# Kernel tuning notes

Hardware: AMD Instinct MI355X
Metric: run time of the kernel (lower is better)

The kernel has to match this reference:

```python
import jax, jax.numpy as jnp
import numpy as np

N = 100000
E = 800000
D_IN = 128
D_H = 128
D_OUT = 40
L = 16
ALPHA = 0.1
THETA = 0.5
BN_EPS = 1e-5


def setup_inputs() -> dict:
    key = jax.random.key(0)
    ks = jax.random.split(key, 8)
    x = jax.random.normal(ks[0], (N, D_IN), dtype=jnp.float32)
    edge_row = jax.random.randint(ks[1], (E,), 0, N, dtype=jnp.int32)
    edge_col = jax.random.randint(ks[2], (E,), 0, N, dtype=jnp.int32)
    edge_weight = jax.random.uniform(ks[3], (E,), dtype=jnp.float32) / 8.0  # ~normalized adj values
    W_in = jax.random.normal(ks[4], (D_IN, D_H), dtype=jnp.float32) / np.sqrt(D_IN)
    b_in = jnp.zeros((D_H,), jnp.float32)
    conv_W = jax.random.normal(ks[5], (L, D_H, D_H), dtype=jnp.float32) / np.sqrt(D_H)
    bn_gamma = jnp.ones((L, D_H), jnp.float32)
    bn_beta = jnp.zeros((L, D_H), jnp.float32)
    W_out = jax.random.normal(ks[6], (D_H, D_OUT), dtype=jnp.float32) / np.sqrt(D_H)
    b_out = jnp.zeros((D_OUT,), jnp.float32)
    return {"x": x, "edge_weight": edge_weight, "W_in": W_in, "b_in": b_in,
            "conv_W": conv_W, "bn_gamma": bn_gamma, "bn_beta": bn_beta,
            "W_out": W_out, "b_out": b_out,
            "edge_row": edge_row, "edge_col": edge_col}


def reference(x, edge_weight, W_in, b_in, conv_W, bn_gamma, bn_beta, W_out, b_out, edge_row, edge_col):
    # input linear + relu (dropout p=0 -> identity)
    x0 = jax.nn.relu(x @ W_in + b_in)            # [N, D_H]
    # GCN2Conv beta coefficients: log(theta/layer + 1), layer = 1..L
    betas = jnp.log(THETA / jnp.arange(1, L + 1, dtype=jnp.float32) + 1.0)

    def spmm(h):
        # out[i] = sum_{e: row[e]=i} w[e] * h[col[e]]
        msgs = edge_weight[:, None] * h[edge_col]     # [E, D_H]
        return jax.ops.segment_sum(msgs, edge_row, num_segments=N)

    def layer(h, params):
        W, g, bb, beta = params
        a = spmm(h)                                   # propagate
        a = (1.0 - ALPHA) * a + ALPHA * x0            # initial-residual mix
        a = (1.0 - beta) * a + beta * (a @ W)         # shared-weights identity mapping
        mu = jnp.mean(a, axis=0)                      # BatchNorm1d (training stats)
        var = jnp.var(a, axis=0)
        a = (a - mu) * jax.lax.rsqrt(var + BN_EPS) * g + bb
        a = a + h                                     # residual
        return jax.nn.relu(a), None

    xL, _ = jax.lax.scan(layer, x0, (conv_W, bn_gamma, bn_beta, betas))
    return xL @ W_out + b_out                         # [N, D_OUT]
```

## Files before the change

kernel.cpp:

```cpp
#include <hip/hip_runtime.h>
#include <math.h>

#define NN 100000
#define EE 800000
#define DH 128
#define NL 16
#define GEMM_GRID 1563
#define SG_GRID 782
#define NSLOT 32
#define WROWS 12500

typedef __bf16 bf16x8 __attribute__((ext_vector_type(8)));
typedef float f32x4 __attribute__((ext_vector_type(4)));

__global__ void k_hist(const int* __restrict__ row, int* __restrict__ cnt) {
    int e = blockIdx.x * 256 + threadIdx.x;
    if (e < EE) atomicAdd(&cnt[row[e]], 1);
}

__global__ void k_scan1(const int* __restrict__ cnt, int* __restrict__ rp, int* __restrict__ part) {
    __shared__ int buf[512];
    int tid = threadIdx.x;
    int i = blockIdx.x * 512 + tid;
    int v = (i < NN) ? cnt[i] : 0;
    buf[tid] = v;
    __syncthreads();
    for (int off = 1; off < 512; off <<= 1) {
        int x = (tid >= off) ? buf[tid - off] : 0;
        __syncthreads();
        buf[tid] += x;
        __syncthreads();
    }
    if (i < NN) rp[i] = buf[tid] - v;
    if (tid == 511) part[blockIdx.x] = buf[511];
}

__global__ void k_scan2(int* __restrict__ part, int nparts) {
    __shared__ int buf[256];
    int tid = threadIdx.x;
    int v = (tid < nparts) ? part[tid] : 0;
    buf[tid] = v;
    __syncthreads();
    for (int off = 1; off < 256; off <<= 1) {
        int x = (tid >= off) ? buf[tid - off] : 0;
        __syncthreads();
        buf[tid] += x;
        __syncthreads();
    }
    if (tid < nparts) part[tid] = buf[tid] - v;
}

__global__ void k_scan3(int* __restrict__ rp, const int* __restrict__ part) {
    int i = blockIdx.x * 512 + threadIdx.x;
    if (i < NN) rp[i] += part[blockIdx.x];
    if (i == 0) rp[NN] = EE;
}

__global__ void k_dhist(const int* __restrict__ cnt, int* __restrict__ dbin) {
    __shared__ int lb[64];
    int tid = threadIdx.x;
    if (tid < 64) lb[tid] = 0;
    __syncthreads();
    int i = blockIdx.x * 256 + tid;
    if (i < NN) {
        int d = cnt[i];
        if (d > 63) d = 63;
        atomicAdd(&lb[63 - d], 1);
    }
    __syncthreads();
    if (tid < 64 && lb[tid]) atomicAdd(&dbin[tid], lb[tid]);
}

__global__ void k_pscan(const int* __restrict__ dbin, int* __restrict__ dpre) {
    if (threadIdx.x == 0) {
        int s = 0;
        for (int i = 0; i < 64; ++i) { dpre[i] = s; s += dbin[i]; }
    }
}

__global__ void k_pscatter(const int* __restrict__ cnt, const int* __restrict__ dpre,
                           int* __restrict__ dfil, int* __restrict__ perm) {
    __shared__ int lcnt[64], lbase[64];
    int tid = threadIdx.x;
    if (tid < 64) lcnt[tid] = 0;
    __syncthreads();
    int i = blockIdx.x * 256 + tid;
    int b = 0, loc = 0;
    bool ok = (i < NN);
    if (ok) {
        int d = cnt[i];
        if (d > 63) d = 63;
        b = 63 - d;
        loc = atomicAdd(&lcnt[b], 1);
    }
    __syncthreads();
    if (tid < 64 && lcnt[tid]) lbase[tid] = atomicAdd(&dfil[tid], lcnt[tid]);
    __syncthreads();
    if (ok) perm[dpre[b] + lbase[b] + loc] = i;
}

__global__ void k_fill(const int* __restrict__ row, const int* __restrict__ col,
                       const float* __restrict__ w, const int* __restrict__ rp,
                       int* __restrict__ fil, int2* __restrict__ ep) {
    int b = blockIdx.x;
    int win = b & 7;
    int e = (b >> 3) * 256 + threadIdx.x;
    if (e >= EE) return;
    int r = row[e];
    if (r / WROWS != win) return;
    int pos = rp[r] + atomicAdd(&fil[r], 1);
    ep[pos] = make_int2(col[e], __float_as_int(0.9f * w[e]));
}

__global__ void k_prep_w(const float* __restrict__ convW, const float* __restrict__ Win,
                         __bf16* __restrict__ Bhi, __bf16* __restrict__ Blo) {
    int l = blockIdx.x;
    const float* W;
    float beta, ob;
    if (l < NL) {
        beta = logf(0.5f / (float)(l + 1) + 1.0f);
        ob = 1.0f - beta;
        W = convW + (size_t)l * DH * DH;
    } else {
        beta = 1.0f;
        ob = 0.0f;
        W = Win;
    }
    __bf16* bh = Bhi + (size_t)l * DH * DH;
    __bf16* bl = Blo + (size_t)l * DH * DH;
    for (int i = threadIdx.x; i < DH * DH; i += 256) {
        int k = i >> 7, j = i & 127;
        float v = beta * W[i] + ((k == j) ? ob : 0.f);
        __bf16 hv = (__bf16)v;
        int t = j >> 4, n = j & 15, ks = k >> 5, quad = (k >> 3) & 3, e = k & 7;
        int off = ((t * 4 + ks) * 64 + quad * 16 + n) * 8 + e;
        bh[off] = hv;
        bl[off] = (__bf16)(v - (float)hv);
    }
}

__global__ void k_prep_out(const float* __restrict__ Wout, __bf16* __restrict__ Bhi, __bf16* __restrict__ Blo) {
    for (int i = threadIdx.x; i < DH * 48; i += 256) {
        int k = i / 48, j = i % 48;
        float v = (j < 40) ? Wout[k * 40 + j] : 0.f;
        __bf16 hv = (__bf16)v;
        int t = j >> 4, n = j & 15, ks = k >> 5, quad = (k >> 3) & 3, e = k & 7;
        int off = ((t * 4 + ks) * 64 + quad * 16 + n) * 8 + e;
        Bhi[off] = hv;
        Blo[off] = (__bf16)(v - (float)hv);
    }
}

__device__ inline void split8(const float* p, bf16x8& hi, bf16x8& lo) {
    f32x4 v0 = *(const f32x4*)p;
    f32x4 v1 = *(const f32x4*)(p + 4);
#pragma unroll
    for (int j = 0; j < 4; ++j) {
        __bf16 h0 = (__bf16)v0[j];
        hi[j] = h0;
        lo[j] = (__bf16)(v0[j] - (float)h0);
        __bf16 h1 = (__bf16)v1[j];
        hi[4 + j] = h1;
        lo[4 + j] = (__bf16)(v1[j] - (float)h1);
    }
}

#define MFMA(a, b, c) __builtin_amdgcn_mfma_f32_16x16x32_bf16(a, b, c, 0, 0, 0)

__device__ inline float dec_scale(unsigned int sc4, int ks) {
    return __uint_as_float(((sc4 >> (8 * ks)) & 0xffu) << 23);
}

#define DEC_DW(dw, wsv, a0, a1, a2, a3)                         \
    {                                                           \
        a0 = fmaf(wsv, (float)((dw)&0xffu), a0);                \
        a1 = fmaf(wsv, (float)(((dw) >> 8) & 0xffu), a1);       \
        a2 = fmaf(wsv, (float)(((dw) >> 16) & 0xffu), a2);      \
        a3 = fmaf(wsv, (float)((dw) >> 24), a3);                \
    }

#define EDGE_FMA(S4, W, RA, RB)                                       \
    {                                                                 \
        float _w = (W);                                               \
        float _w0 = _w * dec_scale(S4, 0);                            \
        float _w1 = _w * dec_scale(S4, 1);                            \
        float _w2 = _w * dec_scale(S4, 2);                            \
        float _w3 = _w * dec_scale(S4, 3);                            \
        sw0 += _w0; sw1 += _w1; sw2 += _w2; sw3 += _w3;               \
        DEC_DW((RA).x, _w0, acc[0][0], acc[0][1], acc[0][2], acc[0][3]); \
        DEC_DW((RA).y, _w0, acc[0][4], acc[0][5], acc[0][6], acc[0][7]); \
        DEC_DW((RA).z, _w1, acc[1][0], acc[1][1], acc[1][2], acc[1][3]); \
        DEC_DW((RA).w, _w1, acc[1][4], acc[1][5], acc[1][6], acc[1][7]); \
        DEC_DW((RB).x, _w2, acc[2][0], acc[2][1], acc[2][2], acc[2][3]); \
        DEC_DW((RB).y, _w2, acc[2][4], acc[2][5], acc[2][6], acc[2][7]); \
        DEC_DW((RB).z, _w3, acc[3][0], acc[3][1], acc[3][2], acc[3][3]); \
        DEC_DW((RB).w, _w3, acc[3][4], acc[3][5], acc[3][6], acc[3][7]); \
    }

__global__ void k_cvt8(const __bf16* __restrict__ src, unsigned char* __restrict__ q8,
                       unsigned char* __restrict__ sc) {
    int t = blockIdx.x * 256 + threadIdx.x;
    if (t >= NN * 4) return;
    int node = t >> 2, ks = t & 3;
    const __bf16* p = src + (size_t)node * DH + ks * 32;
    float v[32];
    float mx = 0.f;
#pragma unroll
    for (int i = 0; i < 4; ++i) {
        bf16x8 b = *(const bf16x8*)(p + i * 8);
#pragma unroll
        for (int c = 0; c < 8; ++c) {
            float f = (float)b[c];
            v[i * 8 + c] = f;
            mx = fmaxf(mx, fabsf(f));
        }
    }
    unsigned int em = (__float_as_uint(mx) >> 23) & 0xffu;
    unsigned int eb;
    float sinv;
    if (em < 7) { eb = 0; sinv = 0.f; }
    else { eb = em - 6; sinv = __uint_as_float((254 - eb) << 23); }
    sc[(size_t)node * 4 + ks] = (unsigned char)eb;
    unsigned char* bp = q8 + (size_t)node * 128 + (ks >> 1) * 64 + (ks & 1) * 8;
#pragma unroll
    for (int q = 0; q < 4; ++q) {
        uint2 w;
        w.x = 0; w.y = 0;
#pragma unroll
        for (int c = 0; c < 4; ++c) {
            unsigned int q0 = (unsigned int)rintf(fminf(fmaf(v[q * 8 + c], sinv, 128.f), 255.f));
            unsigned int q1 = (unsigned int)rintf(fminf(fmaf(v[q * 8 + 4 + c], sinv, 128.f), 255.f));
            w.x |= q0 << (8 * c);
            w.y |= q1 << (8 * c);
        }
        *(uint2*)(bp + q * 16) = w;
    }
}

__global__ __launch_bounds__(512, 4) void k_spmm_gemm(const unsigned char* __restrict__ hin8,
                                                      const unsigned char* __restrict__ hinsc,
                                                      const unsigned char* __restrict__ x08,
                                                      const unsigned char* __restrict__ x0sc,
                                                      const int* __restrict__ rp, const int2* __restrict__ ep,
                                                      const int* __restrict__ perm,
                                                      __bf16* __restrict__ aout,
                                                      const __bf16* __restrict__ Bhi, const __bf16* __restrict__ Blo,
                                                      float* __restrict__ stats32) {
    __shared__ __bf16 Bs[2 * DH * DH];
    __shared__ float red[2][8][DH];
    int tid = threadIdx.x;
    {
        const f32x4* sh = (const f32x4*)Bhi;
        const f32x4* sl = (const f32x4*)Blo;
        f32x4* dh = (f32x4*)Bs;
        f32x4* dl = (f32x4*)(Bs + DH * DH);
#pragma unroll
        for (int i = 0; i < 4; ++i) {
            dh[tid + i * 512] = sh[tid + i * 512];
            dl[tid + i * 512] = sl[tid + i * 512];
        }
    }

    int wave = tid >> 6, lane = tid & 63;
    int n = lane & 15, quad = lane >> 4;
    int r0 = blockIdx.x * 128 + wave * 16;
    int idx = r0 + n;
    int pidx = (idx < NN) ? idx : (NN - 1);
    int node = perm[pidx];

    float acc[4][8];
#pragma unroll
    for (int ks = 0; ks < 4; ++ks)
#pragma unroll
        for (int c = 0; c < 8; ++c) acc[ks][c] = 0.f;
    float sw0 = 0.f, sw1 = 0.f, sw2 = 0.f, sw3 = 0.f;

    unsigned xs4 = *(const unsigned*)&x0sc[(size_t)node * 4];
    const unsigned char* xb = x08 + (size_t)node * 128 + quad * 16;
    uint4 xa = *(const uint4*)xb;
    uint4 xc = *(const uint4*)(xb + 64);

    int s = 0, e = 0;
    if (idx < NN) { s = rp[node]; e = rp[node + 1]; }
    int cnt = e - s;
    int npairs = cnt >> 1;

    const unsigned char* hb = hin8 + quad * 16;

    int2 cP0, cP1, fP0, fP1;
    unsigned cS0, cS1;
    uint4 cA0, cB0, cA1, cB1;
    if (npairs > 0) {
        cP0 = ep[s]; cP1 = ep[s + 1];
        cS0 = *(const unsigned*)&hinsc[(size_t)cP0.x * 4];
        cS1 = *(const unsigned*)&hinsc[(size_t)cP1.x * 4];
        const unsigned char* b0 = hb + (size_t)cP0.x * 128;
        const unsigned char* b1 = hb + (size_t)cP1.x * 128;
        cA0 = *(const uint4*)b0; cB0 = *(const uint4*)(b0 + 64);
        cA1 = *(const uint4*)b1; cB1 = *(const uint4*)(b1 + 64);
        int jf = s + 2; if (jf > EE - 2) jf = EE - 2;
        fP0 = ep[jf]; fP1 = ep[jf + 1];
    }

    EDGE_FMA(xs4, 0.1f, xa, xc);

    int j = s;
    for (int it = 0; it < npairs; ++it) {
        int j2 = j + 4; if (j2 > EE - 2) j2 = EE - 2;
        int2 eN0 = ep[j2], eN1 = ep[j2 + 1];
        unsigned tS0 = *(const unsigned*)&hinsc[(size_t)fP0.x * 4];
        unsigned tS1 = *(const unsigned*)&hinsc[(size_t)fP1.x * 4];
        const unsigned char* b0 = hb + (size_t)fP0.x * 128;
        const unsigned char* b1 = hb + (size_t)fP1.x * 128;
        uint4 tA0 = *(const uint4*)b0, tB0 = *(const uint4*)(b0 + 64);
        uint4 tA1 = *(const uint4*)b1, tB1 = *(const uint4*)(b1 + 64);
        EDGE_FMA(cS0, __int_as_float(cP0.y), cA0, cB0);
        EDGE_FMA(cS1, __int_as_float(cP1.y), cA1, cB1);
        cP0 = fP0; cP1 = fP1; fP0 = eN0; fP1 = eN1;
        cS0 = tS0; cS1 = tS1;
        cA0 = tA0; cB0 = tB0; cA1 = tA1; cB1 = tB1;
        j += 2;
    }
    if (cnt & 1) {
        int2 pe = ep[e - 1];
        unsigned s4 = *(const unsigned*)&hinsc[(size_t)pe.x * 4];
        const unsigned char* bp = hb + (size_t)pe.x * 128;
        uint4 ra = *(const uint4*)bp, rb = *(const uint4*)(bp + 64);
        EDGE_FMA(s4, __int_as_float(pe.y), ra, rb);
    }

    bf16x8 av[4];
    {
        float sws[4] = {sw0, sw1, sw2, sw3};
#pragma unroll
        for (int ks = 0; ks < 4; ++ks)
#pragma unroll
            for (int c = 0; c < 8; ++c)
                av[ks][c] = (__bf16)(acc[ks][c] - 128.0f * sws[ks]);
    }

    int prow[4];
#pragma unroll
    for (int r = 0; r < 4; ++r) prow[r] = __shfl(node, quad * 4 + r);

    __syncthreads();

    f32x4 gacc[8];
#pragma unroll
    for (int t = 0; t < 8; ++t) gacc[t] = (f32x4){0.f, 0.f, 0.f, 0.f};

#pragma unroll
    for (int ks = 0; ks < 4; ++ks) {
#pragma unroll
        for (int t = 0; t < 8; ++t) {
            int base = ((t * 4 + ks) * 64 + lane) * 8;
            bf16x8 bh = *(const bf16x8*)&Bs[base];
            bf16x8 bl = *(const bf16x8*)&Bs[DH * DH + base];
            gacc[t] = MFMA(av[ks], bh, gacc[t]);
            gacc[t] = MFMA(av[ks], bl, gacc[t]);
        }
    }

#pragma unroll
    for (int t = 0; t < 8; ++t) {
        float sm = 0.f, qq = 0.f;
#pragma unroll
        for (int r = 0; r < 4; ++r) {
            int row = r0 + quad * 4 + r;
            float v = gacc[t][r];
            if (row < NN) {
                aout[(size_t)prow[r] * DH + t * 16 + n] = (__bf16)v;
                sm += v;
                qq += v * v;
            }
        }
        sm += __shfl_xor(sm, 16); sm += __shfl_xor(sm, 32);
        qq += __shfl_xor(qq, 16); qq += __shfl_xor(qq, 32);
        if (quad == 0) {
            red[0][wave][t * 16 + n] = sm;
            red[1][wave][t * 16 + n] = qq;
        }
    }
    __syncthreads();
    if (tid < 256) {
        int which = tid >> 7, jj = tid & 127;
        float tot = 0.f;
#pragma unroll
        for (int w = 0; w < 8; ++w) tot += red[which][w][jj];
        atomicAdd(&stats32[(size_t)(blockIdx.x & (NSLOT - 1)) * 256 + tid], tot);
    }
}

__global__ __launch_bounds__(256) void k_lin_in(const float* __restrict__ X,
                                                const __bf16* __restrict__ Bhi, const __bf16* __restrict__ Blo,
                                                const float* __restrict__ bin, __bf16* __restrict__ x0) {
    __shared__ __bf16 Bs[2 * DH * DH];
    int tid = threadIdx.x;
    {
        const f32x4* sh = (const f32x4*)Bhi;
        const f32x4* sl = (const f32x4*)Blo;
        f32x4* dh = (f32x4*)Bs;
        f32x4* dl = (f32x4*)(Bs + DH * DH);
#pragma unroll
        for (int i = 0; i < 8; ++i) {
            dh[tid + i * 256] = sh[tid + i * 256];
            dl[tid + i * 256] = sl[tid + i * 256];
        }
    }
    __syncthreads();

    int wave = tid >> 6, lane = tid & 63;
    int n = lane & 15, quad = lane >> 4;
    int r0 = blockIdx.x * 64 + wave * 16;
    int arow = r0 + n;
    if (arow > NN - 1) arow = NN - 1;
    const float* pa = X + (size_t)arow * DH + quad * 8;

    f32x4 acc[8];
#pragma unroll
    for (int t = 0; t < 8; ++t) acc[t] = (f32x4){0.f, 0.f, 0.f, 0.f};

#pragma unroll
    for (int ks = 0; ks < 4; ++ks) {
        bf16x8 ah, al;
        split8(pa + ks * 32, ah, al);
#pragma unroll
        for (int t = 0; t < 8; ++t) {
            int base = ((t * 4 + ks) * 64 + lane) * 8;
            bf16x8 bh = *(const bf16x8*)&Bs[base];
            bf16x8 bl = *(const bf16x8*)&Bs[DH * DH + base];
            acc[t] = MFMA(ah, bh, acc[t]);
            acc[t] = MFMA(al, bh, acc[t]);
            acc[t] = MFMA(ah, bl, acc[t]);
        }
    }

#pragma unroll
    for (int t = 0; t < 8; ++t) {
        float bj = bin[t * 16 + n];
#pragma unroll
        for (int r = 0; r < 4; ++r) {
            int row = r0 + quad * 4 + r;
            if (row < NN) {
                float v = fmaxf(acc[t][r] + bj, 0.f);
                x0[(size_t)row * DH + t * 16 + n] = (__bf16)v;
            }
        }
    }
}

__global__ __launch_bounds__(256) void k_gemm_out(const __bf16* __restrict__ A,
                                                  const __bf16* __restrict__ Bhi, const __bf16* __restrict__ Blo,
                                                  const float* __restrict__ bout, float* __restrict__ out) {
    __shared__ __bf16 Bs[2 * 48 * DH];
    int tid = threadIdx.x;
    {
        const f32x4* sh = (const f32x4*)Bhi;
        const f32x4* sl = (const f32x4*)Blo;
        f32x4* dh = (f32x4*)Bs;
        f32x4* dl = (f32x4*)(Bs + 48 * DH);
#pragma unroll
        for (int i = 0; i < 3; ++i) {
            dh[tid + i * 256] = sh[tid + i * 256];
            dl[tid + i * 256] = sl[tid + i * 256];
        }
    }
    __syncthreads();

    int wave = tid >> 6, lane = tid & 63;
    int n = lane & 15, quad = lane >> 4;
    int r0 = blockIdx.x * 64 + wave * 16;
    int arow = r0 + n;
    if (arow > NN - 1) arow = NN - 1;
    const __bf16* pa = A + (size_t)arow * DH + quad * 8;

    f32x4 acc[3];
#pragma unroll
    for (int t = 0; t < 3; ++t) acc[t] = (f32x4){0.f, 0.f, 0.f, 0.f};

#pragma unroll
    for (int ks = 0; ks < 4; ++ks) {
        bf16x8 av = *(const bf16x8*)(pa + ks * 32);
#pragma unroll
        for (int t = 0; t < 3; ++t) {
            int base = ((t * 4 + ks) * 64 + lane) * 8;
            bf16x8 bh = *(const bf16x8*)&Bs[base];
            bf16x8 bl = *(const bf16x8*)&Bs[48 * DH + base];
            acc[t] = MFMA(av, bh, acc[t]);
            acc[t] = MFMA(av, bl, acc[t]);
        }
    }

#pragma unroll
    for (int t = 0; t < 3; ++t) {
        int j = t * 16 + n;
        float bj = (j < 40) ? bout[j] : 0.f;
#pragma unroll
        for (int r = 0; r < 4; ++r) {
            int row = r0 + quad * 4 + r;
            if (row < NN && j < 40) out[(size_t)row * 40 + j] = acc[t][r] + bj;
        }
    }
}

__global__ __launch_bounds__(256) void k_update(const __bf16* __restrict__ a, const __bf16* __restrict__ hin,
                                                __bf16* __restrict__ hout,
                                                unsigned char* __restrict__ h8, unsigned char* __restrict__ hsc,
                                                const float* __restrict__ stats32,
                                                const float* __restrict__ gamma, const float* __restrict__ bbeta) {
    __shared__ float scb[DH], shb[DH];
    int tid = threadIdx.x;
    if (tid < DH) {
        float s = 0.f, q = 0.f;
#pragma unroll
        for (int sl = 0; sl < NSLOT; ++sl) {
            s += stats32[(size_t)sl * 256 + tid];
            q += stats32[(size_t)sl * 256 + 128 + tid];
        }
        float mu = s * (1.0f / NN);
        float var = q * (1.0f / NN) - mu * mu;
        if (var < 0.f) var = 0.f;
        float sc = gamma[tid] * rsqrtf(var + 1e-5f);
        scb[tid] = sc;
        shb[tid] = bbeta[tid] - mu * sc;
    }
    __syncthreads();

    int idx = blockIdx.x * 256 + tid;
    int sub = idx & 15;
    int j0 = sub * 8;
    bf16x8 av = ((const bf16x8*)a)[idx];
    bf16x8 hv = ((const bf16x8*)hin)[idx];
    bf16x8 o;
    float vv[8];
    float mx = 0.f;
#pragma unroll
    for (int c = 0; c < 8; ++c) {
        int j = j0 + c;
        float v = fmaxf(fmaf((float)av[c], scb[j], shb[j]) + (float)hv[c], 0.f);
        vv[c] = v;
        mx = fmaxf(mx, v);
        o[c] = (__bf16)v;
    }
    ((bf16x8*)hout)[idx] = o;

    mx = fmaxf(mx, __shfl_xor(mx, 1));
    mx = fmaxf(mx, __shfl_xor(mx, 2));
    unsigned int em = (__float_as_uint(mx) >> 23) & 0xffu;
    unsigned int eb;
    float sinv;
    if (em < 7) { eb = 0; sinv = 0.f; }
    else { eb = em - 6; sinv = __uint_as_float((254 - eb) << 23); }
    if ((tid & 3) == 0) hsc[(size_t)(idx >> 4) * 4 + (sub >> 2)] = (unsigned char)eb;
    uint2 pk;
    pk.x = 0; pk.y = 0;
#pragma unroll
    for (int c = 0; c < 4; ++c) {
        unsigned int q0 = (unsigned int)rintf(fminf(fmaf(vv[c], sinv, 128.f), 255.f));
        unsigned int q1 = (unsigned int)rintf(fminf(fmaf(vv[4 + c], sinv, 128.f), 255.f));
        pk.x |= q0 << (8 * c);
        pk.y |= q1 << (8 * c);
    }
    unsigned wpos = ((sub >> 3) & 1) * 64 + (sub & 3) * 16 + ((sub >> 2) & 1) * 8;
    *(uint2*)&h8[(size_t)(idx >> 4) * 128 + wpos] = pk;
}

extern "C" void kernel_launch(void* const* d_in, const int* in_sizes, int n_in,
                              void* d_out, int out_size, void* d_ws, size_t ws_size,
                              hipStream_t stream) {
    const float* x = (const float*)d_in[0];
    const float* ew = (const float*)d_in[1];
    const float* Win = (const float*)d_in[2];
    const float* bin = (const float*)d_in[3];
    const float* convW = (const float*)d_in[4];
    const float* gamma = (const float*)d_in[5];
    const float* bbeta = (const float*)d_in[6];
    const float* Wout = (const float*)d_in[7];
    const float* bout = (const float*)d_in[8];
    const int* erow = (const int*)d_in[9];
    const int* ecol = (const int*)d_in[10];
    float* out = (float*)d_out;

    char* wsp = (char*)d_ws;
    size_t off = 0;
    auto alloc = [&](size_t bytes) -> void* {
        void* p = wsp + off;
        off += (bytes + 255) & ~(size_t)255;
        return p;
    };
    __bf16* x0 = (__bf16*)alloc((size_t)NN * DH * 2);
    __bf16* h = (__bf16*)alloc((size_t)NN * DH * 2);
    __bf16* a = (__bf16*)alloc((size_t)NN * DH * 2);
    unsigned char* x08 = (unsigned char*)alloc((size_t)NN * DH);
    unsigned char* h8 = (unsigned char*)alloc((size_t)NN * DH);
    unsigned char* x0sc = (unsigned char*)alloc((size_t)NN * 4);
    unsigned char* hsc = (unsigned char*)alloc((size_t)NN * 4);
    int* rp = (int*)alloc((NN + 1) * 4);
    int* perm = (int*)alloc((size_t)NN * 4);
    int* dpre = (int*)alloc(64 * 4);
    size_t zero_bytes = (size_t)NN * 4 + (size_t)NN * 4 + (size_t)NL * NSLOT * 256 * 4 + 128 * 4;
    int* cnt = (int*)alloc(zero_bytes);
    int* fil = cnt + NN;
    float* stats32 = (float*)(fil + NN);
    int* dbin = (int*)(stats32 + (size_t)NL * NSLOT * 256);
    int* dfil = dbin + 64;
    int2* ep = (int2*)alloc((size_t)EE * 8);
    int* part = (int*)alloc(256 * 4);
    __bf16* Bhi = (__bf16*)alloc((size_t)(NL + 1) * DH * DH * 2);
    __bf16* Blo = (__bf16*)alloc((size_t)(NL + 1) * DH * DH * 2);
    __bf16* Bohi = (__bf16*)alloc((size_t)DH * 48 * 2);
    __bf16* Bolo = (__bf16*)alloc((size_t)DH * 48 * 2);

    hipMemsetAsync(cnt, 0, zero_bytes, stream);

    k_hist<<<3125, 256, 0, stream>>>(erow, cnt);
    k_dhist<<<391, 256, 0, stream>>>(cnt, dbin);
    k_pscan<<<1, 64, 0, stream>>>(dbin, dpre);
    k_pscatter<<<391, 256, 0, stream>>>(cnt, dpre, dfil, perm);
    k_scan1<<<196, 512, 0, stream>>>(cnt, rp, part);
    k_scan2<<<1, 256, 0, stream>>>(part, 196);
    k_scan3<<<196, 512, 0, stream>>>(rp, part);
    k_fill<<<25000, 256, 0, stream>>>(erow, ecol, ew, rp, fil, ep);

    k_prep_w<<<NL + 1, 256, 0, stream>>>(convW, Win, Bhi, Blo);
    k_prep_out<<<1, 256, 0, stream>>>(Wout, Bohi, Bolo);

    k_lin_in<<<GEMM_GRID, 256, 0, stream>>>(x, Bhi + (size_t)NL * DH * DH, Blo + (size_t)NL * DH * DH, bin, x0);
    k_cvt8<<<1563, 256, 0, stream>>>(x0, x08, x0sc);

    for (int l = 0; l < NL; ++l) {
        const unsigned char* hin8 = (l == 0) ? x08 : h8;
        const unsigned char* hinsc = (l == 0) ? x0sc : hsc;
        const __bf16* hin = (l == 0) ? x0 : h;
        float* st = stats32 + (size_t)l * NSLOT * 256;
        k_spmm_gemm<<<SG_GRID, 512, 0, stream>>>(hin8, hinsc, x08, x0sc, rp, ep, perm, a,
                                                 Bhi + (size_t)l * DH * DH, Blo + (size_t)l * DH * DH, st);
        k_update<<<6250, 256, 0, stream>>>(a, hin, h, h8, hsc, st, gamma + l * DH, bbeta + l * DH);
    }
    k_gemm_out<<<GEMM_GRID, 256, 0, stream>>>(h, Bohi, Bolo, bout, out);
}
```

Before: 1.174 ms.

## Store node features in degree-sorted order and relabel edges via inverse permutation

Renumbers all nodes into degree-sorted order once at setup: an inverse permutation relabels edge rows and columns, the input linear layer gathers X through perm, and the output GEMM scatters results back to original order. The per-layer spmm kernel then reads its own row, x0 and writes aout contiguously instead of indirecting through perm. This removes the perm lookup and the scattered 128-wide row writes and reads in each of the 16 layers, in exchange for a small extra setup kernel and gathered loads and stores in the input and output GEMMs. Neighbor gathers stay random.

```diff
diff --git a/kernel.cpp b/kernel.cpp
--- a/kernel.cpp
+++ b/kernel.cpp
@@ -99,17 +99,28 @@
     if (ok) perm[dpre[b] + lbase[b] + loc] = i;
 }
 
+__global__ void k_iperm(const int* __restrict__ perm, const int* __restrict__ cnt,
+                        int* __restrict__ iperm, int* __restrict__ cnt2) {
+    int i = blockIdx.x * 256 + threadIdx.x;
+    if (i < NN) {
+        int p = perm[i];
+        iperm[p] = i;
+        cnt2[i] = cnt[p];
+    }
+}
+
 __global__ void k_fill(const int* __restrict__ row, const int* __restrict__ col,
                        const float* __restrict__ w, const int* __restrict__ rp,
+                       const int* __restrict__ iperm,
                        int* __restrict__ fil, int2* __restrict__ ep) {
     int b = blockIdx.x;
     int win = b & 7;
     int e = (b >> 3) * 256 + threadIdx.x;
     if (e >= EE) return;
-    int r = row[e];
+    int r = iperm[row[e]];
     if (r / WROWS != win) return;
     int pos = rp[r] + atomicAdd(&fil[r], 1);
-    ep[pos] = make_int2(col[e], __float_as_int(0.9f * w[e]));
+    ep[pos] = make_int2(iperm[col[e]], __float_as_int(0.9f * w[e]));
 }
 
 __global__ void k_prep_w(const float* __restrict__ convW, const float* __restrict__ Win,
@@ -242,7 +253,6 @@
                                                       const unsigned char* __restrict__ x08,
                                                       const unsigned char* __restrict__ x0sc,
                                                       const int* __restrict__ rp, const int2* __restrict__ ep,
-                                                      const int* __restrict__ perm,
                                                       __bf16* __restrict__ aout,
                                                       const __bf16* __restrict__ Bhi, const __bf16* __restrict__ Blo,
                                                       float* __restrict__ stats32) {
@@ -264,9 +274,8 @@
     int wave = tid >> 6, lane = tid & 63;
     int n = lane & 15, quad = lane >> 4;
     int r0 = blockIdx.x * 128 + wave * 16;
-    int idx = r0 + n;
-    int pidx = (idx < NN) ? idx : (NN - 1);
-    int node = perm[pidx];
+    int node = r0 + n;
+    int nc = (node < NN) ? node : (NN - 1);
 
     float acc[4][8];
 #pragma unroll
@@ -275,13 +284,13 @@
         for (int c = 0; c < 8; ++c) acc[ks][c] = 0.f;
     float sw0 = 0.f, sw1 = 0.f, sw2 = 0.f, sw3 = 0.f;
 
-    unsigned xs4 = *(const unsigned*)&x0sc[(size_t)node * 4];
-    const unsigned char* xb = x08 + (size_t)node * 128 + quad * 16;
+    unsigned xs4 = *(const unsigned*)&x0sc[(size_t)nc * 4];
+    const unsigned char* xb = x08 + (size_t)nc * 128 + quad * 16;
     uint4 xa = *(const uint4*)xb;
     uint4 xc = *(const uint4*)(xb + 64);
 
     int s = 0, e = 0;
-    if (idx < NN) { s = rp[node]; e = rp[node + 1]; }
+    if (node < NN) { s = rp[node]; e = rp[node + 1]; }
     int cnt = e - s;
     int npairs = cnt >> 1;
 
@@ -339,10 +348,6 @@
                 av[ks][c] = (__bf16)(acc[ks][c] - 128.0f * sws[ks]);
     }
 
-    int prow[4];
-#pragma unroll
-    for (int r = 0; r < 4; ++r) prow[r] = __shfl(node, quad * 4 + r);
-
     __syncthreads();
 
     f32x4 gacc[8];
@@ -369,7 +374,7 @@
             int row = r0 + quad * 4 + r;
             float v = gacc[t][r];
             if (row < NN) {
-                aout[(size_t)prow[r] * DH + t * 16 + n] = (__bf16)v;
+                aout[(size_t)row * DH + t * 16 + n] = (__bf16)v;
                 sm += v;
                 qq += v * v;
             }
@@ -391,9 +396,9 @@
     }
 }
 
-__global__ __launch_bounds__(256) void k_lin_in(const float* __restrict__ X,
-                                                const __bf16* __restrict__ Bhi, const __bf16* __restrict__ Blo,
-                                                const float* __restrict__ bin, __bf16* __restrict__ x0) {
+__global__ __launch_bounds__(512, 4) void k_lin_in(const float* __restrict__ X, const int* __restrict__ perm,
+                                                   const __bf16* __restrict__ Bhi, const __bf16* __restrict__ Blo,
+                                                   const float* __restrict__ bin, __bf16* __restrict__ x0) {
     __shared__ __bf16 Bs[2 * DH * DH];
     int tid = threadIdx.x;
     {
@@ -402,19 +407,19 @@
         f32x4* dh = (f32x4*)Bs;
         f32x4* dl = (f32x4*)(Bs + DH * DH);
 #pragma unroll
-        for (int i = 0; i < 8; ++i) {
-            dh[tid + i * 256] = sh[tid + i * 256];
-            dl[tid + i * 256] = sl[tid + i * 256];
+        for (int i = 0; i < 4; ++i) {
+            dh[tid + i * 512] = sh[tid + i * 512];
+            dl[tid + i * 512] = sl[tid + i * 512];
         }
     }
     __syncthreads();
 
     int wave = tid >> 6, lane = tid & 63;
     int n = lane & 15, quad = lane >> 4;
-    int r0 = blockIdx.x * 64 + wave * 16;
+    int r0 = blockIdx.x * 128 + wave * 16;
     int arow = r0 + n;
     if (arow > NN - 1) arow = NN - 1;
-    const float* pa = X + (size_t)arow * DH + quad * 8;
+    const float* pa = X + (size_t)perm[arow] * DH + quad * 8;
 
     f32x4 acc[8];
 #pragma unroll
@@ -449,7 +454,7 @@
     }
 }
 
-__global__ __launch_bounds__(256) void k_gemm_out(const __bf16* __restrict__ A,
+__global__ __launch_bounds__(256) void k_gemm_out(const __bf16* __restrict__ A, const int* __restrict__ perm,
                                                   const __bf16* __restrict__ Bhi, const __bf16* __restrict__ Blo,
                                                   const float* __restrict__ bout, float* __restrict__ out) {
     __shared__ __bf16 Bs[2 * 48 * DH];
@@ -491,6 +496,13 @@
         }
     }
 
+    int prow[4];
+#pragma unroll
+    for (int r = 0; r < 4; ++r) {
+        int row = r0 + quad * 4 + r;
+        prow[r] = (row < NN) ? perm[row] : 0;
+    }
+
 #pragma unroll
     for (int t = 0; t < 3; ++t) {
         int j = t * 16 + n;
@@ -498,7 +510,7 @@
 #pragma unroll
         for (int r = 0; r < 4; ++r) {
             int row = r0 + quad * 4 + r;
-            if (row < NN && j < 40) out[(size_t)row * 40 + j] = acc[t][r] + bj;
+            if (row < NN && j < 40) out[(size_t)prow[r] * 40 + j] = acc[t][r] + bj;
         }
     }
 }
@@ -597,6 +609,8 @@
     unsigned char* hsc = (unsigned char*)alloc((size_t)NN * 4);
     int* rp = (int*)alloc((NN + 1) * 4);
     int* perm = (int*)alloc((size_t)NN * 4);
+    int* iperm = (int*)alloc((size_t)NN * 4);
+    int* cnt2 = (int*)alloc((size_t)NN * 4);
     int* dpre = (int*)alloc(64 * 4);
     size_t zero_bytes = (size_t)NN * 4 + (size_t)NN * 4 + (size_t)NL * NSLOT * 256 * 4 + 128 * 4;
     int* cnt = (int*)alloc(zero_bytes);
@@ -617,15 +631,16 @@
     k_dhist<<<391, 256, 0, stream>>>(cnt, dbin);
     k_pscan<<<1, 64, 0, stream>>>(dbin, dpre);
     k_pscatter<<<391, 256, 0, stream>>>(cnt, dpre, dfil, perm);
-    k_scan1<<<196, 512, 0, stream>>>(cnt, rp, part);
+    k_iperm<<<391, 256, 0, stream>>>(perm, cnt, iperm, cnt2);
+    k_scan1<<<196, 512, 0, stream>>>(cnt2, rp, part);
     k_scan2<<<1, 256, 0, stream>>>(part, 196);
     k_scan3<<<196, 512, 0, stream>>>(rp, part);
-    k_fill<<<25000, 256, 0, stream>>>(erow, ecol, ew, rp, fil, ep);
+    k_fill<<<25000, 256, 0, stream>>>(erow, ecol, ew, rp, iperm, fil, ep);
 
     k_prep_w<<<NL + 1, 256, 0, stream>>>(convW, Win, Bhi, Blo);
     k_prep_out<<<1, 256, 0, stream>>>(Wout, Bohi, Bolo);
 
-    k_lin_in<<<GEMM_GRID, 256, 0, stream>>>(x, Bhi + (size_t)NL * DH * DH, Blo + (size_t)NL * DH * DH, bin, x0);
+    k_lin_in<<<SG_GRID, 512, 0, stream>>>(x, perm, Bhi + (size_t)NL * DH * DH, Blo + (size_t)NL * DH * DH, bin, x0);
     k_cvt8<<<1563, 256, 0, stream>>>(x0, x08, x0sc);
 
     for (int l = 0; l < NL; ++l) {
@@ -633,9 +648,9 @@
         const unsigned char* hinsc = (l == 0) ? x0sc : hsc;
         const __bf16* hin = (l == 0) ? x0 : h;
         float* st = stats32 + (size_t)l * NSLOT * 256;
-        k_spmm_gemm<<<SG_GRID, 512, 0, stream>>>(hin8, hinsc, x08, x0sc, rp, ep, perm, a,
+        k_spmm_gemm<<<SG_GRID, 512, 0, stream>>>(hin8, hinsc, x08, x0sc, rp, ep, a,
                                                  Bhi + (size_t)l * DH * DH, Blo + (size_t)l * DH * DH, st);
         k_update<<<6250, 256, 0, stream>>>(a, hin, h, h8, hsc, st, gamma + l * DH, bbeta + l * DH);
     }
-    k_gemm_out<<<GEMM_GRID, 256, 0, stream>>>(h, Bohi, Bolo, bout, out);
-}
+    k_gemm_out<<<GEMM_GRID, 256, 0, stream>>>(h, perm, Bohi, Bolo, bout, out);
+}
```

Result: no change. 1.154 ms (-1.6%).
